# Performance work log

Measured on AMD Instinct MI355X. Metric: run time of the kernel, lower is better.

## Reference

```python
import jax, jax.numpy as jnp
import numpy as np

B, S, D, H = 4, 2048, 512, 8
DK = D // H
SCALE = 1.0 / np.sqrt(DK)


def setup_inputs() -> dict:
    key = jax.random.key(0)
    kx, kq, kk, kv = jax.random.split(key, 4)
    w_std = np.sqrt(2.0 / (D + D))  # xavier-ish scale
    return {
        "x": jax.random.normal(kx, (B, S, D), dtype=jnp.float32),
        "W_Q": jax.random.normal(kq, (D, D), dtype=jnp.float32) * w_std,
        "W_K": jax.random.normal(kk, (D, D), dtype=jnp.float32) * w_std,
        "W_V": jax.random.normal(kv, (D, D), dtype=jnp.float32) * w_std,
    }


def reference(x, W_Q, W_K, W_V):
    # torch Linear(bias=False): y = x @ W.T
    q = jnp.einsum('bsd,ed->bse', x, W_Q).reshape(B, S, H, DK).transpose(0, 2, 1, 3)
    k = jnp.einsum('bsd,ed->bse', x, W_K).reshape(B, S, H, DK).transpose(0, 2, 1, 3)
    v = jnp.einsum('bsd,ed->bse', x, W_V).reshape(B, S, H, DK).transpose(0, 2, 1, 3)
    scores = jnp.einsum('bhqd,bhkd->bhqk', q, k) * SCALE  # [B,H,S,S]
    scores_exp = jnp.exp(scores)  # faithful: no max-subtraction in original
    attn = scores_exp / (scores_exp.sum(axis=-1, keepdims=True) + 1e-8)
    context = jnp.einsum('bhqk,bhkd->bhqd', attn, v)
    return context.transpose(0, 2, 1, 3).reshape(B, S, D)
```

## Files before the change

kernel.cpp:

```cpp
#include <hip/hip_runtime.h>
#include <hip/hip_bf16.h>

#define Bsz 4
#define Ssz 2048
#define Dsz 512
#define Hsz 8
#define DKsz 64

typedef __bf16 bf16x8 __attribute__((ext_vector_type(8)));
typedef __bf16 bf16x4 __attribute__((ext_vector_type(4)));
typedef float f32x4 __attribute__((ext_vector_type(4)));

#define SWE(c, row) ((((c) ^ ((row) & 7)) * 8))

#define GLL16(g, l) __builtin_amdgcn_global_load_lds(                      \
    (const __attribute__((address_space(1))) void*)(g),                    \
    (__attribute__((address_space(3))) void*)(l), 16, 0, 0)

__global__ __launch_bounds__(256) void cvt_kernel(
    const float* __restrict__ x, const float* __restrict__ Wq,
    const float* __restrict__ Wk, const float* __restrict__ Wv,
    __bf16* __restrict__ xb, __bf16* __restrict__ Wb)
{
    const int i = blockIdx.x * 256 + threadIdx.x;
    const int XN4 = (Bsz * Ssz * Dsz) / 4;
    const float* src;
    __bf16* dst;
    int off;
    if (i < XN4) {
        src = x; dst = xb; off = i;
    } else {
        int j = i - XN4;
        int w = j >> 16;
        off = j & 65535;
        src = (w == 0) ? Wq : (w == 1) ? Wk : Wv;
        dst = Wb + (size_t)w * (Dsz * Dsz);
    }
    float4 v = ((const float4*)src)[off];
    __bf16 o[4] = {(__bf16)v.x, (__bf16)v.y, (__bf16)v.z, (__bf16)v.w};
    *(uint2*)(dst + (size_t)off * 4) = *(uint2*)o;
}

__global__ __launch_bounds__(256, 3) void qkv_kernel(
    const __bf16* __restrict__ xb, const __bf16* __restrict__ Wb,
    __bf16* __restrict__ Qo, __bf16* __restrict__ Ko, __bf16* __restrict__ Vo)
{
    __shared__ __bf16 xs[128][64];
    __shared__ __bf16 wsh[128][64];

    const int tid  = threadIdx.x;
    const int lane = tid & 63;
    const int wave = tid >> 6;
    const int quad = lane >> 4;
    const int l16  = lane & 15;
    const int wm   = (wave & 1) * 64;
    const int wn   = (wave >> 1) * 64;

    const int lin = blockIdx.x;
    const int xcd = lin & 7;
    const int idx = lin >> 3;
    const int tnw = idx % 12;
    const int tmh = idx / 12;
    const int tm  = (tmh * 8 + xcd) * 128;
    const int tn  = (tnw & 3) * 128;
    const int which = tnw >> 2;
    const bool VM = (which == 2);
    const __bf16* W = Wb + (size_t)which * (Dsz * Dsz);

    const int rl  = lane >> 3;
    const int gch = (lane & 7) ^ rl;
    const __bf16* xsrc = xb + (size_t)(tm + wave * 8 + rl) * Dsz + gch * 8;
    const __bf16* wsrc = W  + (size_t)(tn + wave * 8 + rl) * Dsz + gch * 8;

    f32x4 acc[4][4];
    #pragma unroll
    for (int i = 0; i < 4; ++i)
        #pragma unroll
        for (int j = 0; j < 4; ++j) acc[i][j] = (f32x4){0.f, 0.f, 0.f, 0.f};

    const __bf16 (*Ash)[64] = VM ? xs : wsh;
    const __bf16 (*Bsh)[64] = VM ? wsh : xs;

    for (int k0 = 0; k0 < Dsz; k0 += 64) {
        __syncthreads();
        #pragma unroll
        for (int i = 0; i < 4; ++i) {
            GLL16(xsrc + (size_t)(32 * i) * Dsz + k0, &xs[wave * 8 + 32 * i][0]);
            GLL16(wsrc + (size_t)(32 * i) * Dsz + k0, &wsh[wave * 8 + 32 * i][0]);
        }
        asm volatile("s_waitcnt vmcnt(0)" ::: "memory");
        __syncthreads();

        #pragma unroll
        for (int kk = 0; kk < 2; ++kk) {
            bf16x8 fa[4], fb[4];
            #pragma unroll
            for (int mi = 0; mi < 4; ++mi) {
                const int row = wm + mi * 16 + l16;
                fa[mi] = *(const bf16x8*)&Ash[row][SWE(kk * 4 + quad, row)];
            }
            #pragma unroll
            for (int ni = 0; ni < 4; ++ni) {
                const int row = wn + ni * 16 + l16;
                fb[ni] = *(const bf16x8*)&Bsh[row][SWE(kk * 4 + quad, row)];
            }
            #pragma unroll
            for (int mi = 0; mi < 4; ++mi)
                #pragma unroll
                for (int ni = 0; ni < 4; ++ni)
                    acc[mi][ni] = __builtin_amdgcn_mfma_f32_16x16x32_bf16(
                        fa[mi], fb[ni], acc[mi][ni], 0, 0, 0);
        }
    }

    if (!VM) {
        const float scale = (which == 0) ? 0.125f * 1.44269504088896340736f : 1.0f;
        __bf16* dst = (which == 0) ? Qo : Ko;
        #pragma unroll
        for (int mi = 0; mi < 4; ++mi) {
            const int e0 = tn + wm + mi * 16 + quad * 4;
            const int h = e0 >> 6, d0 = e0 & 63;
            #pragma unroll
            for (int ni = 0; ni < 4; ++ni) {
                const int sf = tm + wn + ni * 16 + l16;
                const int b = sf >> 11, s = sf & (Ssz - 1);
                bf16x4 p;
                #pragma unroll
                for (int r = 0; r < 4; ++r) p[r] = (__bf16)(acc[mi][ni][r] * scale);
                *(bf16x4*)&dst[((((size_t)(b * Hsz + h) * Ssz + s)) << 6) + d0] = p;
            }
        }
    } else {
        #pragma unroll
        for (int mi = 0; mi < 4; ++mi) {
            const int sf0 = tm + wm + mi * 16 + quad * 4;
            const int b = sf0 >> 11, s0 = sf0 & (Ssz - 1);
            #pragma unroll
            for (int ni = 0; ni < 4; ++ni) {
                const int e = tn + wn + ni * 16 + l16;
                const int h = e >> 6, d = e & 63;
                bf16x4 p;
                #pragma unroll
                for (int r = 0; r < 4; ++r) p[r] = (__bf16)acc[mi][ni][r];
                *(bf16x4*)&Vo[(((size_t)(b * Hsz + h) * DKsz + d) << 11) + s0] = p;
            }
        }
    }
}

__global__ __launch_bounds__(256, 2) void attn_kernel(
    const __bf16* __restrict__ Q, const __bf16* __restrict__ K,
    const __bf16* __restrict__ VT, float* __restrict__ out)
{
    __shared__ __bf16 ks[2][64][64];
    __shared__ __bf16 vs[2][64][64];
    __shared__ __bf16 psA[4][16][64];
    __shared__ __bf16 psB[4][16][64];

    const int tid  = threadIdx.x;
    const int lane = tid & 63;
    const int wave = tid >> 6;
    const int quad = lane >> 4;
    const int l16  = lane & 15;

    const int bh = blockIdx.x;
    const int qt = blockIdx.y;
    const int b  = bh >> 3;
    const int h  = bh & 7;

    const __bf16* Qb = Q  + (size_t)bh * Ssz * DKsz;
    const __bf16* Kb = K  + (size_t)bh * Ssz * DKsz;
    const __bf16* Vb = VT + (size_t)bh * DKsz * Ssz;

    bf16x8 qf[2][2];
    #pragma unroll
    for (int qs = 0; qs < 2; ++qs) {
        const __bf16* qrow = Qb + (size_t)(qt * 128 + wave * 32 + qs * 16 + l16) * DKsz;
        qf[qs][0] = *(const bf16x8*)(qrow + quad * 8);
        qf[qs][1] = *(const bf16x8*)(qrow + 32 + quad * 8);
    }

    bf16x8 ones;
    #pragma unroll
    for (int i = 0; i < 8; ++i) ones[i] = (__bf16)1.0f;

    f32x4 oacc[2][4];
    #pragma unroll
    for (int qs = 0; qs < 2; ++qs)
        #pragma unroll
        for (int i = 0; i < 4; ++i) oacc[qs][i] = (f32x4){0.f, 0.f, 0.f, 0.f};
    f32x4 lacc[2] = {(f32x4){0.f, 0.f, 0.f, 0.f}, (f32x4){0.f, 0.f, 0.f, 0.f}};

    const int rl  = lane >> 3;
    const int gch = (lane & 7) ^ rl;

#define STAGE_KV(DST, KBASE)                                                   \
    do {                                                                       \
        const __bf16* kgs = Kb + (size_t)((KBASE) + wave * 8 + rl) * DKsz      \
                               + gch * 8;                                      \
        const __bf16* vgs = Vb + (size_t)(wave * 8 + rl) * Ssz + (KBASE)       \
                               + gch * 8;                                      \
        GLL16(kgs,                        &ks[DST][wave * 8][0]);              \
        GLL16(kgs + (size_t)32 * DKsz,    &ks[DST][wave * 8 + 32][0]);         \
        GLL16(vgs,                        &vs[DST][wave * 8][0]);              \
        GLL16(vgs + (size_t)32 * Ssz,     &vs[DST][wave * 8 + 32][0]);         \
    } while (0)

    STAGE_KV(0, 0);
    asm volatile("s_waitcnt vmcnt(0)\n\ts_barrier" ::: "memory");

#define ATTN_TILE(CUR, KB)                                                     \
    do {                                                                       \
        if ((KB) + 64 < Ssz) STAGE_KV((CUR) ^ 1, (KB) + 64);                   \
        bf16x8 kf[2][4], vf[2][4];                                             \
        _Pragma("unroll")                                                      \
        for (int kk = 0; kk < 2; ++kk)                                         \
            _Pragma("unroll")                                                  \
            for (int ns = 0; ns < 4; ++ns) {                                   \
                const int row = ns * 16 + l16;                                 \
                kf[kk][ns] = *(const bf16x8*)&ks[CUR][row][SWE(kk*4+quad,row)];\
                vf[kk][ns] = *(const bf16x8*)&vs[CUR][row][SWE(kk*4+quad,row)];\
            }                                                                  \
        __builtin_amdgcn_s_setprio(1);                                         \
        f32x4 st[2][4];                                                        \
        _Pragma("unroll")                                                      \
        for (int qs = 0; qs < 2; ++qs)                                         \
            _Pragma("unroll")                                                  \
            for (int ns = 0; ns < 4; ++ns) {                                   \
                f32x4 t = (f32x4){0.f, 0.f, 0.f, 0.f};                         \
                t = __builtin_amdgcn_mfma_f32_16x16x32_bf16(                   \
                        kf[0][ns], qf[qs][0], t, 0, 0, 0);                     \
                t = __builtin_amdgcn_mfma_f32_16x16x32_bf16(                   \
                        kf[1][ns], qf[qs][1], t, 0, 0, 0);                     \
                st[qs][ns] = t;                                                \
            }                                                                  \
        __builtin_amdgcn_s_setprio(0);                                         \
        _Pragma("unroll")                                                      \
        for (int qs = 0; qs < 2; ++qs)                                         \
            _Pragma("unroll")                                                  \
            for (int ns = 0; ns < 4; ++ns) {                                   \
                bf16x4 pp;                                                     \
                _Pragma("unroll")                                              \
                for (int r = 0; r < 4; ++r)                                    \
                    pp[r] = (__bf16)__builtin_amdgcn_exp2f(st[qs][ns][r]);     \
                __bf16* pbase = qs ? &psB[wave][l16][0] : &psA[wave][l16][0];  \
                const int c = ns * 2 + (quad >> 1);                            \
                *(bf16x4*)&pbase[((c ^ (l16 & 7)) << 3) + ((quad & 1) << 2)]   \
                    = pp;                                                      \
            }                                                                  \
        bf16x8 af[2][2];                                                       \
        af[0][0] = *(const bf16x8*)&psA[wave][l16][SWE(quad, l16)];            \
        af[0][1] = *(const bf16x8*)&psA[wave][l16][SWE(4 + quad, l16)];        \
        af[1][0] = *(const bf16x8*)&psB[wave][l16][SWE(quad, l16)];            \
        af[1][1] = *(const bf16x8*)&psB[wave][l16][SWE(4 + quad, l16)];        \
        __builtin_amdgcn_s_setprio(1);                                         \
        _Pragma("unroll")                                                      \
        for (int qs = 0; qs < 2; ++qs) {                                       \
            _Pragma("unroll")                                                  \
            for (int ns = 0; ns < 4; ++ns) {                                   \
                oacc[qs][ns] = __builtin_amdgcn_mfma_f32_16x16x32_bf16(        \
                    vf[0][ns], af[qs][0], oacc[qs][ns], 0, 0, 0);              \
                oacc[qs][ns] = __builtin_amdgcn_mfma_f32_16x16x32_bf16(        \
                    vf[1][ns], af[qs][1], oacc[qs][ns], 0, 0, 0);              \
            }                                                                  \
            lacc[qs] = __builtin_amdgcn_mfma_f32_16x16x32_bf16(                \
                ones, af[qs][0], lacc[qs], 0, 0, 0);                           \
            lacc[qs] = __builtin_amdgcn_mfma_f32_16x16x32_bf16(                \
                ones, af[qs][1], lacc[qs], 0, 0, 0);                           \
        }                                                                      \
        __builtin_amdgcn_s_setprio(0);                                         \
        asm volatile("s_waitcnt vmcnt(0) lgkmcnt(0)\n\ts_barrier"              \
                     ::: "memory");                                           \
    } while (0)

    for (int kb = 0; kb < Ssz; kb += 128) {
        ATTN_TILE(0, kb);
        ATTN_TILE(1, kb + 64);
    }

    #pragma unroll
    for (int qs = 0; qs < 2; ++qs) {
        const float linv = 1.f / (lacc[qs][0] + 1e-8f);
        const int q = qt * 128 + wave * 32 + qs * 16 + l16;
        float* obase = out + ((size_t)b * Ssz + q) * Dsz + h * DKsz;
        #pragma unroll
        for (int ns = 0; ns < 4; ++ns) {
            f32x4 o = oacc[qs][ns] * linv;
            *(f32x4*)(obase + ns * 16 + quad * 4) = o;
        }
    }
#undef ATTN_TILE
#undef STAGE_KV
}

extern "C" void kernel_launch(void* const* d_in, const int* in_sizes, int n_in,
                              void* d_out, int out_size, void* d_ws, size_t ws_size,
                              hipStream_t stream) {
    const float* x  = (const float*)d_in[0];
    const float* Wq = (const float*)d_in[1];
    const float* Wk = (const float*)d_in[2];
    const float* Wv = (const float*)d_in[3];
    float* out = (float*)d_out;

    const size_t per = (size_t)Bsz * Hsz * Ssz * DKsz;
    __bf16* Qw  = (__bf16*)d_ws;
    __bf16* Kw  = Qw + per;
    __bf16* VTw = Kw + per;
    __bf16* xb  = VTw + per;
    __bf16* Wb  = xb + per;

    cvt_kernel<<<4864, 256, 0, stream>>>(x, Wq, Wk, Wv, xb, Wb);
    qkv_kernel<<<768, 256, 0, stream>>>(xb, Wb, Qw, Kw, VTw);
    attn_kernel<<<dim3(Bsz * Hsz, Ssz / 128), 256, 0, stream>>>(Qw, Kw, VTw, out);
}
```

Before: 139.8 us.

## Double attention query tile per block to 256 rows to reuse K/V loads

Each wave now handles 64 query rows (four 16-row subtiles) instead of 32, so a block covers 256 queries and the grid halves. Every K/V tile staged in shared memory is reused across twice as many queries, which cuts global K/V traffic and barrier overhead per unit of work. The per-subtile loop interleaves QK MFMA, exp and PV MFMA. In exchange it raises register pressure (launch bounds drop to 1 block per SIMD group) and leaves only 256 blocks, which may underfill the GPU's CUs.

```diff
diff --git a/kernel.cpp b/kernel.cpp
--- a/kernel.cpp
+++ b/kernel.cpp
@@ -148,14 +148,13 @@
     }
 }
 
-__global__ __launch_bounds__(256, 2) void attn_kernel(
+__global__ __launch_bounds__(256, 1) void attn_kernel(
     const __bf16* __restrict__ Q, const __bf16* __restrict__ K,
     const __bf16* __restrict__ VT, float* __restrict__ out)
 {
     __shared__ __bf16 ks[2][64][64];
     __shared__ __bf16 vs[2][64][64];
-    __shared__ __bf16 psA[4][16][64];
-    __shared__ __bf16 psB[4][16][64];
+    __shared__ __bf16 ps[4][4][16][64];
 
     const int tid  = threadIdx.x;
     const int lane = tid & 63;
@@ -172,10 +171,10 @@
     const __bf16* Kb = K  + (size_t)bh * Ssz * DKsz;
     const __bf16* Vb = VT + (size_t)bh * DKsz * Ssz;
 
-    bf16x8 qf[2][2];
-    #pragma unroll
-    for (int qs = 0; qs < 2; ++qs) {
-        const __bf16* qrow = Qb + (size_t)(qt * 128 + wave * 32 + qs * 16 + l16) * DKsz;
+    bf16x8 qf[4][2];
+    #pragma unroll
+    for (int qs = 0; qs < 4; ++qs) {
+        const __bf16* qrow = Qb + (size_t)(qt * 256 + wave * 64 + qs * 16 + l16) * DKsz;
         qf[qs][0] = *(const bf16x8*)(qrow + quad * 8);
         qf[qs][1] = *(const bf16x8*)(qrow + 32 + quad * 8);
     }
@@ -184,12 +183,14 @@
     #pragma unroll
     for (int i = 0; i < 8; ++i) ones[i] = (__bf16)1.0f;
 
-    f32x4 oacc[2][4];
-    #pragma unroll
-    for (int qs = 0; qs < 2; ++qs)
+    f32x4 oacc[4][4];
+    #pragma unroll
+    for (int qs = 0; qs < 4; ++qs)
         #pragma unroll
         for (int i = 0; i < 4; ++i) oacc[qs][i] = (f32x4){0.f, 0.f, 0.f, 0.f};
-    f32x4 lacc[2] = {(f32x4){0.f, 0.f, 0.f, 0.f}, (f32x4){0.f, 0.f, 0.f, 0.f}};
+    f32x4 lacc[4];
+    #pragma unroll
+    for (int qs = 0; qs < 4; ++qs) lacc[qs] = (f32x4){0.f, 0.f, 0.f, 0.f};
 
     const int rl  = lane >> 3;
     const int gch = (lane & 7) ^ rl;
@@ -221,10 +222,10 @@
                 kf[kk][ns] = *(const bf16x8*)&ks[CUR][row][SWE(kk*4+quad,row)];\
                 vf[kk][ns] = *(const bf16x8*)&vs[CUR][row][SWE(kk*4+quad,row)];\
             }                                                                  \
-        __builtin_amdgcn_s_setprio(1);                                         \
-        f32x4 st[2][4];                                                        \
         _Pragma("unroll")                                                      \
-        for (int qs = 0; qs < 2; ++qs)                                         \
+        for (int qs = 0; qs < 4; ++qs) {                                       \
+            __builtin_amdgcn_s_setprio(1);                                     \
+            f32x4 st[4];                                                       \
             _Pragma("unroll")                                                  \
             for (int ns = 0; ns < 4; ++ns) {                                   \
                 f32x4 t = (f32x4){0.f, 0.f, 0.f, 0.f};                         \
@@ -232,45 +233,39 @@
                         kf[0][ns], qf[qs][0], t, 0, 0, 0);                     \
                 t = __builtin_amdgcn_mfma_f32_16x16x32_bf16(                   \
                         kf[1][ns], qf[qs][1], t, 0, 0, 0);                     \
-                st[qs][ns] = t;                                                \
+                st[ns] = t;                                                    \
             }                                                                  \
-        __builtin_amdgcn_s_setprio(0);                                         \
-        _Pragma("unroll")                                                      \
-        for (int qs = 0; qs < 2; ++qs)                                         \
+            __builtin_amdgcn_s_setprio(0);                                     \
             _Pragma("unroll")                                                  \
             for (int ns = 0; ns < 4; ++ns) {                                   \
                 bf16x4 pp;                                                     \
                 _Pragma("unroll")                                              \
                 for (int r = 0; r < 4; ++r)                                    \
-                    pp[r] = (__bf16)__builtin_amdgcn_exp2f(st[qs][ns][r]);     \
-                __bf16* pbase = qs ? &psB[wave][l16][0] : &psA[wave][l16][0];  \
+                    pp[r] = (__bf16)__builtin_amdgcn_exp2f(st[ns][r]);         \
                 const int c = ns * 2 + (quad >> 1);                            \
-                *(bf16x4*)&pbase[((c ^ (l16 & 7)) << 3) + ((quad & 1) << 2)]   \
-                    = pp;                                                      \
+                *(bf16x4*)&ps[wave][qs][l16]                                   \
+                    [((c ^ (l16 & 7)) << 3) + ((quad & 1) << 2)] = pp;         \
             }                                                                  \
-        bf16x8 af[2][2];                                                       \
-        af[0][0] = *(const bf16x8*)&psA[wave][l16][SWE(quad, l16)];            \
-        af[0][1] = *(const bf16x8*)&psA[wave][l16][SWE(4 + quad, l16)];        \
-        af[1][0] = *(const bf16x8*)&psB[wave][l16][SWE(quad, l16)];            \
-        af[1][1] = *(const bf16x8*)&psB[wave][l16][SWE(4 + quad, l16)];        \
-        __builtin_amdgcn_s_setprio(1);                                         \
-        _Pragma("unroll")                                                      \
-        for (int qs = 0; qs < 2; ++qs) {                                       \
+            const bf16x8 af0 = *(const bf16x8*)&ps[wave][qs][l16]              \
+                                   [SWE(quad, l16)];                           \
+            const bf16x8 af1 = *(const bf16x8*)&ps[wave][qs][l16]              \
+                                   [SWE(4 + quad, l16)];                       \
+            __builtin_amdgcn_s_setprio(1);                                     \
             _Pragma("unroll")                                                  \
             for (int ns = 0; ns < 4; ++ns) {                                   \
                 oacc[qs][ns] = __builtin_amdgcn_mfma_f32_16x16x32_bf16(        \
-                    vf[0][ns], af[qs][0], oacc[qs][ns], 0, 0, 0);              \
+                    vf[0][ns], af0, oacc[qs][ns], 0, 0, 0);                    \
                 oacc[qs][ns] = __builtin_amdgcn_mfma_f32_16x16x32_bf16(        \
-                    vf[1][ns], af[qs][1], oacc[qs][ns], 0, 0, 0);              \
+                    vf[1][ns], af1, oacc[qs][ns], 0, 0, 0);                    \
             }                                                                  \
             lacc[qs] = __builtin_amdgcn_mfma_f32_16x16x32_bf16(                \
-                ones, af[qs][0], lacc[qs], 0, 0, 0);                           \
+                ones, af0, lacc[qs], 0, 0, 0);                                 \
             lacc[qs] = __builtin_amdgcn_mfma_f32_16x16x32_bf16(                \
-                ones, af[qs][1], lacc[qs], 0, 0, 0);                           \
+                ones, af1, lacc[qs], 0, 0, 0);                                 \
+            __builtin_amdgcn_s_setprio(0);                                     \
         }                                                                      \
-        __builtin_amdgcn_s_setprio(0);                                         \
         asm volatile("s_waitcnt vmcnt(0) lgkmcnt(0)\n\ts_barrier"              \
-                     ::: "memory");                                           \
+                     ::: "memory");                                            \
     } while (0)
 
     for (int kb = 0; kb < Ssz; kb += 128) {
@@ -279,9 +274,9 @@
     }
 
     #pragma unroll
-    for (int qs = 0; qs < 2; ++qs) {
+    for (int qs = 0; qs < 4; ++qs) {
         const float linv = 1.f / (lacc[qs][0] + 1e-8f);
-        const int q = qt * 128 + wave * 32 + qs * 16 + l16;
+        const int q = qt * 256 + wave * 64 + qs * 16 + l16;
         float* obase = out + ((size_t)b * Ssz + q) * Dsz + h * DKsz;
         #pragma unroll
         for (int ns = 0; ns < 4; ++ns) {
@@ -311,5 +306,5 @@
 
     cvt_kernel<<<4864, 256, 0, stream>>>(x, Wq, Wk, Wv, xb, Wb);
     qkv_kernel<<<768, 256, 0, stream>>>(xb, Wb, Qw, Kw, VTw);
-    attn_kernel<<<dim3(Bsz * Hsz, Ssz / 128), 256, 0, stream>>>(Qw, Kw, VTw, out);
+    attn_kernel<<<dim3(Bsz * Hsz, Ssz / 256), 256, 0, stream>>>(Qw, Kw, VTw, out);
 }
```

New measurement: 161.7 us. +15.7%, slower.

## Fuse fp32-to-bf16 conversion into QKV projection with register-prefetched staging

Applied to the files above, without the earlier changes.

Removes the separate conversion kernel. The QKV GEMM now loads fp32 x and W straight from global memory, converts them to bf16 in registers and writes them into swizzled LDS. The next k-tile is prefetched into registers while the current tile is computed, replacing the async global-to-LDS loads. This drops one launch and the bf16 write and read round trip, but each GEMM block now reads fp32 (twice the bytes, re-read across tiles) and uses more registers.

```diff
diff --git a/kernel.cpp b/kernel.cpp
--- a/kernel.cpp
+++ b/kernel.cpp
@@ -17,32 +17,16 @@
     (const __attribute__((address_space(1))) void*)(g),                    \
     (__attribute__((address_space(3))) void*)(l), 16, 0, 0)
 
-__global__ __launch_bounds__(256) void cvt_kernel(
+__device__ inline bf16x8 cvt8(float4 a, float4 b) {
+    bf16x8 r;
+    r[0] = (__bf16)a.x; r[1] = (__bf16)a.y; r[2] = (__bf16)a.z; r[3] = (__bf16)a.w;
+    r[4] = (__bf16)b.x; r[5] = (__bf16)b.y; r[6] = (__bf16)b.z; r[7] = (__bf16)b.w;
+    return r;
+}
+
+__global__ __launch_bounds__(256, 3) void qkv_kernel(
     const float* __restrict__ x, const float* __restrict__ Wq,
     const float* __restrict__ Wk, const float* __restrict__ Wv,
-    __bf16* __restrict__ xb, __bf16* __restrict__ Wb)
-{
-    const int i = blockIdx.x * 256 + threadIdx.x;
-    const int XN4 = (Bsz * Ssz * Dsz) / 4;
-    const float* src;
-    __bf16* dst;
-    int off;
-    if (i < XN4) {
-        src = x; dst = xb; off = i;
-    } else {
-        int j = i - XN4;
-        int w = j >> 16;
-        off = j & 65535;
-        src = (w == 0) ? Wq : (w == 1) ? Wk : Wv;
-        dst = Wb + (size_t)w * (Dsz * Dsz);
-    }
-    float4 v = ((const float4*)src)[off];
-    __bf16 o[4] = {(__bf16)v.x, (__bf16)v.y, (__bf16)v.z, (__bf16)v.w};
-    *(uint2*)(dst + (size_t)off * 4) = *(uint2*)o;
-}
-
-__global__ __launch_bounds__(256, 3) void qkv_kernel(
-    const __bf16* __restrict__ xb, const __bf16* __restrict__ Wb,
     __bf16* __restrict__ Qo, __bf16* __restrict__ Ko, __bf16* __restrict__ Vo)
 {
     __shared__ __bf16 xs[128][64];
@@ -65,12 +49,23 @@
     const int tn  = (tnw & 3) * 128;
     const int which = tnw >> 2;
     const bool VM = (which == 2);
-    const __bf16* W = Wb + (size_t)which * (Dsz * Dsz);
-
-    const int rl  = lane >> 3;
-    const int gch = (lane & 7) ^ rl;
-    const __bf16* xsrc = xb + (size_t)(tm + wave * 8 + rl) * Dsz + gch * 8;
-    const __bf16* wsrc = W  + (size_t)(tn + wave * 8 + rl) * Dsz + gch * 8;
+    const float* W = (which == 0) ? Wq : (which == 1) ? Wk : Wv;
+
+    const int srow = tid >> 3;
+    const int sc   = tid & 7;
+    const int swz  = SWE(sc, srow);
+
+    const float* xg = x + (size_t)(tm + srow) * Dsz + sc * 8;
+    const float* wg = W + (size_t)(tn + srow) * Dsz + sc * 8;
+
+    bf16x8 px[4], pw[4];
+    #pragma unroll
+    for (int i = 0; i < 4; ++i) {
+        px[i] = cvt8(*(const float4*)(xg + (size_t)(32 * i) * Dsz),
+                     *(const float4*)(xg + (size_t)(32 * i) * Dsz + 4));
+        pw[i] = cvt8(*(const float4*)(wg + (size_t)(32 * i) * Dsz),
+                     *(const float4*)(wg + (size_t)(32 * i) * Dsz + 4));
+    }
 
     f32x4 acc[4][4];
     #pragma unroll
@@ -85,11 +80,19 @@
         __syncthreads();
         #pragma unroll
         for (int i = 0; i < 4; ++i) {
-            GLL16(xsrc + (size_t)(32 * i) * Dsz + k0, &xs[wave * 8 + 32 * i][0]);
-            GLL16(wsrc + (size_t)(32 * i) * Dsz + k0, &wsh[wave * 8 + 32 * i][0]);
-        }
-        asm volatile("s_waitcnt vmcnt(0)" ::: "memory");
+            *(bf16x8*)&xs[srow + 32 * i][swz]  = px[i];
+            *(bf16x8*)&wsh[srow + 32 * i][swz] = pw[i];
+        }
         __syncthreads();
+        if (k0 + 64 < Dsz) {
+            #pragma unroll
+            for (int i = 0; i < 4; ++i) {
+                px[i] = cvt8(*(const float4*)(xg + (size_t)(32 * i) * Dsz + k0 + 64),
+                             *(const float4*)(xg + (size_t)(32 * i) * Dsz + k0 + 68));
+                pw[i] = cvt8(*(const float4*)(wg + (size_t)(32 * i) * Dsz + k0 + 64),
+                             *(const float4*)(wg + (size_t)(32 * i) * Dsz + k0 + 68));
+            }
+        }
 
         #pragma unroll
         for (int kk = 0; kk < 2; ++kk) {
@@ -306,10 +309,7 @@
     __bf16* Qw  = (__bf16*)d_ws;
     __bf16* Kw  = Qw + per;
     __bf16* VTw = Kw + per;
-    __bf16* xb  = VTw + per;
-    __bf16* Wb  = xb + per;
-
-    cvt_kernel<<<4864, 256, 0, stream>>>(x, Wq, Wk, Wv, xb, Wb);
-    qkv_kernel<<<768, 256, 0, stream>>>(xb, Wb, Qw, Kw, VTw);
+
+    qkv_kernel<<<768, 256, 0, stream>>>(x, Wq, Wk, Wv, Qw, Kw, VTw);
     attn_kernel<<<dim3(Bsz * Hsz, Ssz / 128), 256, 0, stream>>>(Qw, Kw, VTw, out);
 }
```

After: 144.1 us. 1.03x slower.
